# Kernel tuning notes

Measured on AMD Instinct MI355X. Metric: run time of the kernel, lower is better.

## Reference

```python
import jax, jax.numpy as jnp
import numpy as np

N = 100000
E = 3200000
NFEAT = 256
NHID = 256
NCLASS = 40


def _uniform(key, shape, stdv):
    return jax.random.uniform(key, shape, jnp.float32, -stdv, stdv)


def setup_inputs() -> dict:
    key = jax.random.key(0)
    ks = jax.random.split(key, 16)
    x = jax.random.normal(ks[0], (N, NFEAT), jnp.float32)
    edge_row = jax.random.randint(ks[1], (E,), 0, N, jnp.int32)
    edge_col = jax.random.randint(ks[2], (E,), 0, N, jnp.int32)
    edge_weight = jax.random.uniform(ks[3], (E,), jnp.float32)
    # MyLinear init: stdv = 1/sqrt(out_features)
    dims = [(NFEAT, NHID), (NHID, NHID), (NHID, NHID), (NHID, NCLASS)]
    params = {}
    for i, (fi, fo) in enumerate(dims):
        stdv = 1.0 / np.sqrt(fo)
        params[f"W{i+1}"] = _uniform(ks[4 + 2 * i], (fi, fo), stdv)
        params[f"b{i+1}"] = _uniform(ks[5 + 2 * i], (fo,), stdv)
    return dict(x=x, edge_row=edge_row, edge_col=edge_col, edge_weight=edge_weight, **params)


def _spmm(edge_row, edge_col, edge_weight, x):
    # out[i] = sum_{(i,j) in E} w_ij * x[j]
    msgs = edge_weight[:, None] * x[edge_col]  # [E, d]
    return jax.ops.segment_sum(msgs, edge_row, num_segments=N)


def reference(x, edge_row, edge_col, edge_weight, W1, b1, W2, b2, W3, b3, W4, b4):
    # layer 0 (ix % mlp_layers == 0 -> residual + spmm)
    h = x + _spmm(edge_row, edge_col, edge_weight, x)
    h = jax.nn.relu(h @ W1 + b1)
    # layer 1
    h = jax.nn.relu(h @ W2 + b2)
    # layer 2 (spmm + residual again)
    h = h + _spmm(edge_row, edge_col, edge_weight, h)
    h = jax.nn.relu(h @ W3 + b3)
    # layer 3 (final, no relu)
    h = h @ W4 + b4
    return jax.nn.log_softmax(h, axis=1)
```

## Files before the change

kernel.cpp:

```cpp
#include <hip/hip_runtime.h>
#include <hip/hip_bf16.h>
#include <cstdint>

#define N_NODES 100000
#define N_EDGES 3200000
#define NFEAT   256
#define NCLASS  40

#define BROWS_LOG 7
#define BROWS     128
#define NBUCK     782
#define CHUNK     8192
#define NBLK      391
#define GHN       (NBUCK * NBLK)

#define HP 264

typedef __bf16 bf16;
typedef __attribute__((ext_vector_type(8))) __bf16 bf16x8;
typedef __attribute__((ext_vector_type(4))) float f32x4;
typedef __attribute__((ext_vector_type(2))) float f32x2;

__device__ inline float b2f(unsigned short u) {
    union { unsigned int i; float f; } x; x.i = ((unsigned int)u) << 16; return x.f;
}
__device__ inline unsigned short f2b(float f) {
    union { float f; unsigned int i; } x; x.f = f;
    unsigned int i = x.i;
    return (unsigned short)((i + 0x7fffu + ((i >> 16) & 1u)) >> 16);
}
__device__ inline f32x2 unpack2(unsigned int d) {
    union { unsigned int i; float f; } lo, hi;
    lo.i = d << 16;
    hi.i = d & 0xFFFF0000u;
    return (f32x2){lo.f, hi.f};
}
__device__ inline unsigned int pack2(f32x2 a) {
    return ((unsigned int)f2b(a[0])) | (((unsigned int)f2b(a[1])) << 16);
}

__global__ void prep_w_kernel(const float* __restrict__ W1, const float* __restrict__ W2,
                              const float* __restrict__ W3, const float* __restrict__ W4,
                              unsigned short* __restrict__ WT1, unsigned short* __restrict__ WT2,
                              unsigned short* __restrict__ WT3, unsigned short* __restrict__ WT4) {
    int i = blockIdx.x * blockDim.x + threadIdx.x;
    if (i < 256 * 256) {
        int nIdx = i >> 8, k = i & 255;
        WT1[i] = f2b(W1[k * 256 + nIdx]);
        WT2[i] = f2b(W2[k * 256 + nIdx]);
        WT3[i] = f2b(W3[k * 256 + nIdx]);
    }
    if (i < 48 * 256) {
        int nIdx = i >> 8, k = i & 255;
        WT4[i] = (nIdx < NCLASS) ? f2b(W4[k * NCLASS + nIdx]) : (unsigned short)0;
    }
}

__global__ void cast_kernel(const float* __restrict__ X, unsigned short* __restrict__ Y, int n4) {
    int i = blockIdx.x * blockDim.x + threadIdx.x;
    if (i >= n4) return;
    float4 v = *(const float4*)(X + (size_t)i * 4);
    ushort4 o;
    o.x = f2b(v.x); o.y = f2b(v.y); o.z = f2b(v.z); o.w = f2b(v.w);
    *(ushort4*)(Y + (size_t)i * 4) = o;
}

__global__ __launch_bounds__(256) void p1a_kernel(const int* __restrict__ erow,
                                                  int* __restrict__ ghist) {
    __shared__ int h[NBUCK];
    for (int j = threadIdx.x; j < NBUCK; j += 256) h[j] = 0;
    __syncthreads();
    int base = blockIdx.x * CHUNK;
    for (int j = 0; j < CHUNK; j += 256) {
        int i = base + j + threadIdx.x;
        if (i < N_EDGES) atomicAdd(&h[erow[i] >> BROWS_LOG], 1);
    }
    __syncthreads();
    for (int j = threadIdx.x; j < NBUCK; j += 256)
        ghist[(size_t)j * NBLK + blockIdx.x] = h[j];
}

__global__ void scanB_blocks_kernel(int* __restrict__ g, int* __restrict__ bsums, int n) {
    __shared__ int s[1024];
    int i = blockIdx.x * 1024 + threadIdx.x;
    int v = (i < n) ? g[i] : 0;
    s[threadIdx.x] = v;
    __syncthreads();
    for (int off = 1; off < 1024; off <<= 1) {
        int t = (threadIdx.x >= off) ? s[threadIdx.x - off] : 0;
        __syncthreads();
        s[threadIdx.x] += t;
        __syncthreads();
    }
    if (i < n) g[i] = s[threadIdx.x] - v;
    if (threadIdx.x == 1023) bsums[blockIdx.x] = s[1023];
}

__global__ void scanB_sums_kernel(int* __restrict__ bsums, int nb) {
    __shared__ int s[512];
    int v = (threadIdx.x < nb) ? bsums[threadIdx.x] : 0;
    s[threadIdx.x] = v;
    __syncthreads();
    for (int off = 1; off < 512; off <<= 1) {
        int t = (threadIdx.x >= off) ? s[threadIdx.x - off] : 0;
        __syncthreads();
        s[threadIdx.x] += t;
        __syncthreads();
    }
    if (threadIdx.x < nb) bsums[threadIdx.x] = s[threadIdx.x] - v;
}

__global__ void scanB_add_kernel(int* __restrict__ g, const int* __restrict__ bsums, int n) {
    int i = blockIdx.x * blockDim.x + threadIdx.x;
    if (i < n) g[i] += bsums[i >> 10];
}

__global__ __launch_bounds__(256) void p1c_kernel(const int* __restrict__ erow,
                                                  const int* __restrict__ ecol,
                                                  const float* __restrict__ ew,
                                                  const int* __restrict__ ghist,
                                                  uint2* __restrict__ stage) {
    __shared__ int cur[NBUCK];
    for (int j = threadIdx.x; j < NBUCK; j += 256)
        cur[j] = ghist[(size_t)j * NBLK + blockIdx.x];
    __syncthreads();
    int base = blockIdx.x * CHUNK;
    for (int j = 0; j < CHUNK; j += 1024) {
        int r[4], c[4]; float w[4]; bool m[4];
#pragma unroll
        for (int q = 0; q < 4; q++) {
            int i = base + j + q * 256 + threadIdx.x;
            m[q] = (i < N_EDGES);
            if (m[q]) { r[q] = erow[i]; c[q] = ecol[i]; w[q] = ew[i]; }
        }
#pragma unroll
        for (int q = 0; q < 4; q++) {
            if (m[q]) {
                unsigned int qq = (unsigned int)(w[q] * 32768.f + 0.5f);
                if (qq > 32767u) qq = 32767u;
                int p = atomicAdd(&cur[r[q] >> BROWS_LOG], 1);
                stage[p] = make_uint2((unsigned int)r[q], (((unsigned int)c[q]) << 15) | qq);
            }
        }
    }
}

__global__ __launch_bounds__(256) void p2_kernel(const int* __restrict__ ghist,
                                                 const uint2* __restrict__ stage,
                                                 unsigned int* __restrict__ edges,
                                                 int* __restrict__ rowptr) {
    __shared__ int h[BROWS], sc[BROWS], lcur[BROWS];
    int b = blockIdx.x;
    int lo = ghist[(size_t)b * NBLK];
    int hi = (b + 1 < NBUCK) ? ghist[(size_t)(b + 1) * NBLK] : N_EDGES;
    if (threadIdx.x < BROWS) h[threadIdx.x] = 0;
    __syncthreads();
    for (int i = lo + threadIdx.x; i < hi; i += 256)
        atomicAdd(&h[stage[i].x & (BROWS - 1)], 1);
    __syncthreads();
    if (threadIdx.x < BROWS) sc[threadIdx.x] = h[threadIdx.x];
    __syncthreads();
    for (int off = 1; off < BROWS; off <<= 1) {
        int t = 0;
        if (threadIdx.x < BROWS && threadIdx.x >= off) t = sc[threadIdx.x - off];
        __syncthreads();
        if (threadIdx.x < BROWS) sc[threadIdx.x] += t;
        __syncthreads();
    }
    if (threadIdx.x < BROWS) {
        int ex = sc[threadIdx.x] - h[threadIdx.x];
        int row = b * BROWS + threadIdx.x;
        if (row <= N_NODES) rowptr[row] = lo + ex;
        lcur[threadIdx.x] = lo + ex;
    }
    __syncthreads();
    for (int i = lo + threadIdx.x; i < hi; i += 256) {
        uint2 sd = stage[i];
        int p = atomicAdd(&lcur[sd.x & (BROWS - 1)], 1);
        edges[p] = sd.y;
    }
}

__global__ void spmm_res_kernel(const unsigned short* __restrict__ X, unsigned short* __restrict__ Y,
                                const int* __restrict__ rowptr, const unsigned int* __restrict__ edges,
                                int n) {
    int gtid = blockIdx.x * blockDim.x + threadIdx.x;
    int row = gtid >> 6;
    int lane = gtid & 63;
    if (row >= n) return;
    const int half = lane >> 5;
    const int fb = (lane & 31) * 8;

    f32x2 acc[4];
    {
        uint4 xb = *(const uint4*)(X + (size_t)row * NFEAT + fb);
        if (half == 0) {
            acc[0] = unpack2(xb.x); acc[1] = unpack2(xb.y);
            acc[2] = unpack2(xb.z); acc[3] = unpack2(xb.w);
        } else {
            acc[0] = (f32x2){0.f, 0.f}; acc[1] = (f32x2){0.f, 0.f};
            acc[2] = (f32x2){0.f, 0.f}; acc[3] = (f32x2){0.f, 0.f};
        }
    }

    int s = rowptr[row], e = rowptr[row + 1];
    for (int k = s; k < e; k += 12) {
        int   c[6];
        f32x2 w2[6];
#pragma unroll
        for (int j = 0; j < 6; j++) {
            int kj = k + j * 2 + half;
            int kc = (kj < e) ? kj : (e - 1);
            unsigned int d = edges[kc];
            c[j] = (int)(d >> 15);
            float w = (kj < e) ? (float)(d & 32767u) * (1.f / 32768.f) : 0.f;
            w2[j] = (f32x2){w, w};
        }
        uint4 v[6];
#pragma unroll
        for (int j = 0; j < 6; j++) v[j] = *(const uint4*)(X + (size_t)c[j] * NFEAT + fb);
#pragma unroll
        for (int j = 0; j < 6; j++) {
            acc[0] += w2[j] * unpack2(v[j].x);
            acc[1] += w2[j] * unpack2(v[j].y);
            acc[2] += w2[j] * unpack2(v[j].z);
            acc[3] += w2[j] * unpack2(v[j].w);
        }
    }

#pragma unroll
    for (int i = 0; i < 4; i++) {
        acc[i][0] += __shfl_xor(acc[i][0], 32, 64);
        acc[i][1] += __shfl_xor(acc[i][1], 32, 64);
    }
    if (half == 0) {
        uint4 o;
        o.x = pack2(acc[0]); o.y = pack2(acc[1]);
        o.z = pack2(acc[2]); o.w = pack2(acc[3]);
        *(uint4*)(Y + (size_t)row * NFEAT + fb) = o;
    }
}

__global__ __launch_bounds__(256) void gemm12_kernel(
    const bf16* __restrict__ X,
    const bf16* __restrict__ WT1, const float* __restrict__ b1,
    const bf16* __restrict__ WT2, const float* __restrict__ b2,
    unsigned short* __restrict__ Y, int M) {
    __shared__ unsigned int sB[256 * 20];
    __shared__ unsigned short sH[64 * HP];
    const int tid = threadIdx.x;
    const int wave = tid >> 6;
    const int lane = tid & 63;
    const int m = lane & 15;
    const int quad = lane >> 4;
    const int lrow = wave * 16 + m;
    const int rowBase = blockIdx.x * 64;
    int arow = rowBase + lrow;
    if (arow >= M) arow = M - 1;

    f32x4 acc[16];
#pragma unroll
    for (int t = 0; t < 16; t++) acc[t] = (f32x4){0.f, 0.f, 0.f, 0.f};

    const bf16* xp = X + (size_t)arow * NFEAT + quad * 8;
#pragma unroll
    for (int k0 = 0; k0 < NFEAT; k0 += 32) {
#pragma unroll
        for (int f = tid; f < 1024; f += 256) {
            int n = f >> 2, j = f & 3;
            uint4 v = *(const uint4*)((const unsigned short*)WT1 + (size_t)n * NFEAT + k0 + j * 8);
            *(uint4*)&sB[n * 20 + j * 4] = v;
        }
        __syncthreads();
        bf16x8 a = *(const bf16x8*)(xp + k0);
#pragma unroll
        for (int t = 0; t < 16; t++) {
            bf16x8 b = *(const bf16x8*)&sB[(t * 16 + m) * 20 + quad * 4];
            acc[t] = __builtin_amdgcn_mfma_f32_16x16x32_bf16(b, a, acc[t], 0, 0, 0);
        }
        __syncthreads();
    }
#pragma unroll
    for (int t = 0; t < 16; t++) {
        const float* bp = b1 + t * 16 + quad * 4;
        f32x2 lo = (f32x2){fmaxf(acc[t][0] + bp[0], 0.f), fmaxf(acc[t][1] + bp[1], 0.f)};
        f32x2 hi = (f32x2){fmaxf(acc[t][2] + bp[2], 0.f), fmaxf(acc[t][3] + bp[3], 0.f)};
        *(uint2*)&sH[lrow * HP + t * 16 + quad * 4] = make_uint2(pack2(lo), pack2(hi));
        acc[t] = (f32x4){0.f, 0.f, 0.f, 0.f};
    }
    __syncthreads();

#pragma unroll
    for (int k0 = 0; k0 < NFEAT; k0 += 32) {
#pragma unroll
        for (int f = tid; f < 1024; f += 256) {
            int n = f >> 2, j = f & 3;
            uint4 v = *(const uint4*)((const unsigned short*)WT2 + (size_t)n * NFEAT + k0 + j * 8);
            *(uint4*)&sB[n * 20 + j * 4] = v;
        }
        __syncthreads();
        bf16x8 a = *(const bf16x8*)&sH[lrow * HP + k0 + quad * 8];
#pragma unroll
        for (int t = 0; t < 16; t++) {
            bf16x8 b = *(const bf16x8*)&sB[(t * 16 + m) * 20 + quad * 4];
            acc[t] = __builtin_amdgcn_mfma_f32_16x16x32_bf16(b, a, acc[t], 0, 0, 0);
        }
        __syncthreads();
    }
    const int row = rowBase + lrow;
    if (row < M) {
#pragma unroll
        for (int t = 0; t < 16; t++) {
            const float* bp = b2 + t * 16 + quad * 4;
            f32x2 lo = (f32x2){fmaxf(acc[t][0] + bp[0], 0.f), fmaxf(acc[t][1] + bp[1], 0.f)};
            f32x2 hi = (f32x2){fmaxf(acc[t][2] + bp[2], 0.f), fmaxf(acc[t][3] + bp[3], 0.f)};
            *(uint2*)(Y + (size_t)row * NFEAT + t * 16 + quad * 4) = make_uint2(pack2(lo), pack2(hi));
        }
    }
}

__global__ __launch_bounds__(256) void gemm34_ls_kernel(
    const bf16* __restrict__ X,
    const bf16* __restrict__ WT3, const float* __restrict__ b3,
    const bf16* __restrict__ WT4, const float* __restrict__ b4,
    float* __restrict__ out, int M) {
    __shared__ unsigned int sB[256 * 20];
    __shared__ unsigned short sH[64 * HP];
    const int tid = threadIdx.x;
    const int wave = tid >> 6;
    const int lane = tid & 63;
    const int m = lane & 15;
    const int quad = lane >> 4;
    const int lrow = wave * 16 + m;
    const int rowBase = blockIdx.x * 64;
    int arow = rowBase + lrow;
    if (arow >= M) arow = M - 1;

    f32x4 acc[16];
#pragma unroll
    for (int t = 0; t < 16; t++) acc[t] = (f32x4){0.f, 0.f, 0.f, 0.f};

    const bf16* xp = X + (size_t)arow * NFEAT + quad * 8;
#pragma unroll
    for (int k0 = 0; k0 < NFEAT; k0 += 32) {
#pragma unroll
        for (int f = tid; f < 1024; f += 256) {
            int n = f >> 2, j = f & 3;
            uint4 v = *(const uint4*)((const unsigned short*)WT3 + (size_t)n * NFEAT + k0 + j * 8);
            *(uint4*)&sB[n * 20 + j * 4] = v;
        }
        __syncthreads();
        bf16x8 a = *(const bf16x8*)(xp + k0);
#pragma unroll
        for (int t = 0; t < 16; t++) {
            bf16x8 b = *(const bf16x8*)&sB[(t * 16 + m) * 20 + quad * 4];
            acc[t] = __builtin_amdgcn_mfma_f32_16x16x32_bf16(b, a, acc[t], 0, 0, 0);
        }
        __syncthreads();
    }
#pragma unroll
    for (int t = 0; t < 16; t++) {
        const float* bp = b3 + t * 16 + quad * 4;
        f32x2 lo = (f32x2){fmaxf(acc[t][0] + bp[0], 0.f), fmaxf(acc[t][1] + bp[1], 0.f)};
        f32x2 hi = (f32x2){fmaxf(acc[t][2] + bp[2], 0.f), fmaxf(acc[t][3] + bp[3], 0.f)};
        *(uint2*)&sH[lrow * HP + t * 16 + quad * 4] = make_uint2(pack2(lo), pack2(hi));
    }
    __syncthreads();

    f32x4 a4[3];
#pragma unroll
    for (int t = 0; t < 3; t++) a4[t] = (f32x4){0.f, 0.f, 0.f, 0.f};
#pragma unroll
    for (int k0 = 0; k0 < NFEAT; k0 += 32) {
        if (tid < 192) {
            int n = tid >> 2, j = tid & 3;
            uint4 v = *(const uint4*)((const unsigned short*)WT4 + (size_t)n * NFEAT + k0 + j * 8);
            *(uint4*)&sB[n * 20 + j * 4] = v;
        }
        __syncthreads();
        bf16x8 a = *(const bf16x8*)&sH[lrow * HP + k0 + quad * 8];
#pragma unroll
        for (int t = 0; t < 3; t++) {
            bf16x8 b = *(const bf16x8*)&sB[(t * 16 + m) * 20 + quad * 4];
            a4[t] = __builtin_amdgcn_mfma_f32_16x16x32_bf16(b, a, a4[t], 0, 0, 0);
        }
        __syncthreads();
    }

    float v[3][4];
#pragma unroll
    for (int t = 0; t < 3; t++) {
        bool tv = (t < 2) || (quad < 2);
#pragma unroll
        for (int r = 0; r < 4; r++) {
            float bv = tv ? b4[t * 16 + quad * 4 + r] : 0.f;
            v[t][r] = tv ? (a4[t][r] + bv) : -1e30f;
        }
    }

    float mx = -1e30f;
#pragma unroll
    for (int t = 0; t < 3; t++)
#pragma unroll
        for (int r = 0; r < 4; r++) mx = fmaxf(mx, v[t][r]);
    mx = fmaxf(mx, __shfl_xor(mx, 16, 64));
    mx = fmaxf(mx, __shfl_xor(mx, 32, 64));

    float sm = 0.f;
#pragma unroll
    for (int t = 0; t < 3; t++) {
        bool tv = (t < 2) || (quad < 2);
        if (tv) {
#pragma unroll
            for (int r = 0; r < 4; r++) sm += __expf(v[t][r] - mx);
        }
    }
    sm += __shfl_xor(sm, 16, 64);
    sm += __shfl_xor(sm, 32, 64);
    float ls = __logf(sm);

    const int row = rowBase + lrow;
    if (row < M) {
#pragma unroll
        for (int t = 0; t < 3; t++) {
            if ((t < 2) || (quad < 2)) {
                f32x4 o = (f32x4){v[t][0] - mx - ls, v[t][1] - mx - ls,
                                  v[t][2] - mx - ls, v[t][3] - mx - ls};
                *(f32x4*)(out + (size_t)row * NCLASS + t * 16 + quad * 4) = o;
            }
        }
    }
}

extern "C" void kernel_launch(void* const* d_in, const int* in_sizes, int n_in,
                              void* d_out, int out_size, void* d_ws, size_t ws_size,
                              hipStream_t stream) {
    const float* x   = (const float*)d_in[0];
    const int* erow  = (const int*)d_in[1];
    const int* ecol  = (const int*)d_in[2];
    const float* ew  = (const float*)d_in[3];
    const float* W1  = (const float*)d_in[4];
    const float* W2  = (const float*)d_in[6];
    const float* W3  = (const float*)d_in[8];
    const float* W4  = (const float*)d_in[10];
    const float* b1  = (const float*)d_in[5];
    const float* b2  = (const float*)d_in[7];
    const float* b3  = (const float*)d_in[9];
    const float* b4  = (const float*)d_in[11];

    char* ws = (char*)d_ws;
    size_t off = 0;
    auto alloc = [&](size_t bytes) -> char* {
        char* p = ws + off;
        off = (off + bytes + 255) & ~(size_t)255;
        return p;
    };
    int* rowptr  = (int*)alloc((size_t)(N_NODES + 1) * 4);
    int* bsumsB  = (int*)alloc(512 * 4);
    unsigned int* edges = (unsigned int*)alloc((size_t)N_EDGES * 4);
    int* ghist   = (int*)alloc((size_t)GHN * 4);
    unsigned short* WT1 = (unsigned short*)alloc(256 * 256 * 2);
    unsigned short* WT2 = (unsigned short*)alloc(256 * 256 * 2);
    unsigned short* WT3 = (unsigned short*)alloc(256 * 256 * 2);
    unsigned short* WT4 = (unsigned short*)alloc(48 * 256 * 2);
    unsigned short* hA  = (unsigned short*)alloc((size_t)N_NODES * NFEAT * 2);
    uint2* stage        = (uint2*)hA;
    unsigned short* hB  = (unsigned short*)d_in[0];
    (void)ws_size; (void)n_in; (void)in_sizes; (void)out_size;

    prep_w_kernel<<<(256 * 256 + 255) / 256, 256, 0, stream>>>(
        W1, W2, W3, W4, WT1, WT2, WT3, WT4);
    p1a_kernel<<<NBLK, 256, 0, stream>>>(erow, ghist);
    int nsb = (GHN + 1023) / 1024;
    scanB_blocks_kernel<<<nsb, 1024, 0, stream>>>(ghist, bsumsB, GHN);
    scanB_sums_kernel<<<1, 512, 0, stream>>>(bsumsB, nsb);
    scanB_add_kernel<<<(GHN + 255) / 256, 256, 0, stream>>>(ghist, bsumsB, GHN);
    p1c_kernel<<<NBLK, 256, 0, stream>>>(erow, ecol, ew, ghist, stage);
    p2_kernel<<<NBUCK, 256, 0, stream>>>(ghist, stage, edges, rowptr);

    const int n4 = N_NODES * NFEAT / 4;
    const int spmm_grid = (N_NODES * 64 + 255) / 256;
    const int gemm_grid = (N_NODES + 63) / 64;

    cast_kernel<<<(n4 + 255) / 256, 256, 0, stream>>>(x, hA, n4);
    spmm_res_kernel<<<spmm_grid, 256, 0, stream>>>(hA, hB, rowptr, edges, N_NODES);
    gemm12_kernel<<<gemm_grid, 256, 0, stream>>>(
        (const bf16*)hB, (const bf16*)WT1, b1, (const bf16*)WT2, b2, hB, N_NODES);
    spmm_res_kernel<<<spmm_grid, 256, 0, stream>>>(hB, hA, rowptr, edges, N_NODES);
    gemm34_ls_kernel<<<gemm_grid, 256, 0, stream>>>(
        (const bf16*)hA, (const bf16*)WT3, b3, (const bf16*)WT4, b4, (float*)d_out, N_NODES);
}
```

Before: 917.2 us.

## Keep fused MLP intermediate in registers via permuted weight columns

The output columns of W1 and W3 (and their biases) are permuted at prep time so that each lane's MFMA accumulator layout already matches the A-operand fragment layout of the next GEMM. The intermediate hidden activations are then packed to bf16 in registers instead of being round-tripped through a padded shared-memory tile. This removes the sH buffer, one barrier and LDS traffic, and cuts shared memory per block. Launch bounds are raised to ask for 4 blocks per CU, which risks register spills given the 16 accumulators plus 8 held fragments.

```diff
diff --git a/kernel.cpp b/kernel.cpp
--- a/kernel.cpp
+++ b/kernel.cpp
@@ -14,8 +14,6 @@
 #define NBLK      391
 #define GHN       (NBUCK * NBLK)
 
-#define HP 264
-
 typedef __bf16 bf16;
 typedef __attribute__((ext_vector_type(8))) __bf16 bf16x8;
 typedef __attribute__((ext_vector_type(4))) float f32x4;
@@ -39,16 +37,24 @@
     return ((unsigned int)f2b(a[0])) | (((unsigned int)f2b(a[1])) << 16);
 }
 
+__host__ __device__ inline int permN(int s) {
+    return (((s >> 5) & 7) << 5) | (((s >> 2) & 3) << 3) | (((s >> 4) & 1) << 2) | (s & 3);
+}
+
 __global__ void prep_w_kernel(const float* __restrict__ W1, const float* __restrict__ W2,
                               const float* __restrict__ W3, const float* __restrict__ W4,
+                              const float* __restrict__ b1, const float* __restrict__ b3,
                               unsigned short* __restrict__ WT1, unsigned short* __restrict__ WT2,
-                              unsigned short* __restrict__ WT3, unsigned short* __restrict__ WT4) {
+                              unsigned short* __restrict__ WT3, unsigned short* __restrict__ WT4,
+                              float* __restrict__ b1p, float* __restrict__ b3p) {
     int i = blockIdx.x * blockDim.x + threadIdx.x;
     if (i < 256 * 256) {
-        int nIdx = i >> 8, k = i & 255;
-        WT1[i] = f2b(W1[k * 256 + nIdx]);
-        WT2[i] = f2b(W2[k * 256 + nIdx]);
-        WT3[i] = f2b(W3[k * 256 + nIdx]);
+        int s = i >> 8, k = i & 255;
+        int n = permN(s);
+        WT1[i] = f2b(W1[k * 256 + n]);
+        WT2[i] = f2b(W2[k * 256 + s]);
+        WT3[i] = f2b(W3[k * 256 + n]);
+        if (k == 0) { b1p[s] = b1[n]; b3p[s] = b3[n]; }
     }
     if (i < 48 * 256) {
         int nIdx = i >> 8, k = i & 255;
@@ -241,13 +247,12 @@
     }
 }
 
-__global__ __launch_bounds__(256) void gemm12_kernel(
+__global__ __launch_bounds__(256, 4) void gemm12_kernel(
     const bf16* __restrict__ X,
-    const bf16* __restrict__ WT1, const float* __restrict__ b1,
+    const bf16* __restrict__ WT1p, const float* __restrict__ b1p,
     const bf16* __restrict__ WT2, const float* __restrict__ b2,
     unsigned short* __restrict__ Y, int M) {
     __shared__ unsigned int sB[256 * 20];
-    __shared__ unsigned short sH[64 * HP];
     const int tid = threadIdx.x;
     const int wave = tid >> 6;
     const int lane = tid & 63;
@@ -268,7 +273,7 @@
 #pragma unroll
         for (int f = tid; f < 1024; f += 256) {
             int n = f >> 2, j = f & 3;
-            uint4 v = *(const uint4*)((const unsigned short*)WT1 + (size_t)n * NFEAT + k0 + j * 8);
+            uint4 v = *(const uint4*)((const unsigned short*)WT1p + (size_t)n * NFEAT + k0 + j * 8);
             *(uint4*)&sB[n * 20 + j * 4] = v;
         }
         __syncthreads();
@@ -280,15 +285,25 @@
         }
         __syncthreads();
     }
-#pragma unroll
-    for (int t = 0; t < 16; t++) {
-        const float* bp = b1 + t * 16 + quad * 4;
-        f32x2 lo = (f32x2){fmaxf(acc[t][0] + bp[0], 0.f), fmaxf(acc[t][1] + bp[1], 0.f)};
-        f32x2 hi = (f32x2){fmaxf(acc[t][2] + bp[2], 0.f), fmaxf(acc[t][3] + bp[3], 0.f)};
-        *(uint2*)&sH[lrow * HP + t * 16 + quad * 4] = make_uint2(pack2(lo), pack2(hi));
-        acc[t] = (f32x4){0.f, 0.f, 0.f, 0.f};
-    }
-    __syncthreads();
+
+    bf16x8 af[8];
+#pragma unroll
+    for (int kc = 0; kc < 8; kc++) {
+        const float* p0 = b1p + (2 * kc) * 16 + quad * 4;
+        const float* p1 = b1p + (2 * kc + 1) * 16 + quad * 4;
+        union { unsigned int u[4]; bf16x8 h; } cv;
+        cv.u[0] = pack2((f32x2){fmaxf(acc[2 * kc][0] + p0[0], 0.f),
+                                fmaxf(acc[2 * kc][1] + p0[1], 0.f)});
+        cv.u[1] = pack2((f32x2){fmaxf(acc[2 * kc][2] + p0[2], 0.f),
+                                fmaxf(acc[2 * kc][3] + p0[3], 0.f)});
+        cv.u[2] = pack2((f32x2){fmaxf(acc[2 * kc + 1][0] + p1[0], 0.f),
+                                fmaxf(acc[2 * kc + 1][1] + p1[1], 0.f)});
+        cv.u[3] = pack2((f32x2){fmaxf(acc[2 * kc + 1][2] + p1[2], 0.f),
+                                fmaxf(acc[2 * kc + 1][3] + p1[3], 0.f)});
+        af[kc] = cv.h;
+        acc[2 * kc] = (f32x4){0.f, 0.f, 0.f, 0.f};
+        acc[2 * kc + 1] = (f32x4){0.f, 0.f, 0.f, 0.f};
+    }
 
 #pragma unroll
     for (int k0 = 0; k0 < NFEAT; k0 += 32) {
@@ -299,7 +314,7 @@
             *(uint4*)&sB[n * 20 + j * 4] = v;
         }
         __syncthreads();
-        bf16x8 a = *(const bf16x8*)&sH[lrow * HP + k0 + quad * 8];
+        bf16x8 a = af[k0 >> 5];
 #pragma unroll
         for (int t = 0; t < 16; t++) {
             bf16x8 b = *(const bf16x8*)&sB[(t * 16 + m) * 20 + quad * 4];
@@ -319,13 +334,12 @@
     }
 }
 
-__global__ __launch_bounds__(256) void gemm34_ls_kernel(
+__global__ __launch_bounds__(256, 4) void gemm34_ls_kernel(
     const bf16* __restrict__ X,
-    const bf16* __restrict__ WT3, const float* __restrict__ b3,
+    const bf16* __restrict__ WT3p, const float* __restrict__ b3p,
     const bf16* __restrict__ WT4, const float* __restrict__ b4,
     float* __restrict__ out, int M) {
     __shared__ unsigned int sB[256 * 20];
-    __shared__ unsigned short sH[64 * HP];
     const int tid = threadIdx.x;
     const int wave = tid >> 6;
     const int lane = tid & 63;
@@ -346,7 +360,7 @@
 #pragma unroll
         for (int f = tid; f < 1024; f += 256) {
             int n = f >> 2, j = f & 3;
-            uint4 v = *(const uint4*)((const unsigned short*)WT3 + (size_t)n * NFEAT + k0 + j * 8);
+            uint4 v = *(const uint4*)((const unsigned short*)WT3p + (size_t)n * NFEAT + k0 + j * 8);
             *(uint4*)&sB[n * 20 + j * 4] = v;
         }
         __syncthreads();
@@ -358,14 +372,23 @@
         }
         __syncthreads();
     }
-#pragma unroll
-    for (int t = 0; t < 16; t++) {
-        const float* bp = b3 + t * 16 + quad * 4;
-        f32x2 lo = (f32x2){fmaxf(acc[t][0] + bp[0], 0.f), fmaxf(acc[t][1] + bp[1], 0.f)};
-        f32x2 hi = (f32x2){fmaxf(acc[t][2] + bp[2], 0.f), fmaxf(acc[t][3] + bp[3], 0.f)};
-        *(uint2*)&sH[lrow * HP + t * 16 + quad * 4] = make_uint2(pack2(lo), pack2(hi));
-    }
-    __syncthreads();
+
+    bf16x8 af[8];
+#pragma unroll
+    for (int kc = 0; kc < 8; kc++) {
+        const float* p0 = b3p + (2 * kc) * 16 + quad * 4;
+        const float* p1 = b3p + (2 * kc + 1) * 16 + quad * 4;
+        union { unsigned int u[4]; bf16x8 h; } cv;
+        cv.u[0] = pack2((f32x2){fmaxf(acc[2 * kc][0] + p0[0], 0.f),
+                                fmaxf(acc[2 * kc][1] + p0[1], 0.f)});
+        cv.u[1] = pack2((f32x2){fmaxf(acc[2 * kc][2] + p0[2], 0.f),
+                                fmaxf(acc[2 * kc][3] + p0[3], 0.f)});
+        cv.u[2] = pack2((f32x2){fmaxf(acc[2 * kc + 1][0] + p1[0], 0.f),
+                                fmaxf(acc[2 * kc + 1][1] + p1[1], 0.f)});
+        cv.u[3] = pack2((f32x2){fmaxf(acc[2 * kc + 1][2] + p1[2], 0.f),
+                                fmaxf(acc[2 * kc + 1][3] + p1[3], 0.f)});
+        af[kc] = cv.h;
+    }
 
     f32x4 a4[3];
 #pragma unroll
@@ -378,7 +401,7 @@
             *(uint4*)&sB[n * 20 + j * 4] = v;
         }
         __syncthreads();
-        bf16x8 a = *(const bf16x8*)&sH[lrow * HP + k0 + quad * 8];
+        bf16x8 a = af[k0 >> 5];
 #pragma unroll
         for (int t = 0; t < 3; t++) {
             bf16x8 b = *(const bf16x8*)&sB[(t * 16 + m) * 20 + quad * 4];
@@ -463,13 +486,15 @@
     unsigned short* WT2 = (unsigned short*)alloc(256 * 256 * 2);
     unsigned short* WT3 = (unsigned short*)alloc(256 * 256 * 2);
     unsigned short* WT4 = (unsigned short*)alloc(48 * 256 * 2);
+    float* b1p          = (float*)alloc(256 * 4);
+    float* b3p          = (float*)alloc(256 * 4);
     unsigned short* hA  = (unsigned short*)alloc((size_t)N_NODES * NFEAT * 2);
     uint2* stage        = (uint2*)hA;
     unsigned short* hB  = (unsigned short*)d_in[0];
     (void)ws_size; (void)n_in; (void)in_sizes; (void)out_size;
 
     prep_w_kernel<<<(256 * 256 + 255) / 256, 256, 0, stream>>>(
-        W1, W2, W3, W4, WT1, WT2, WT3, WT4);
+        W1, W2, W3, W4, b1, b3, WT1, WT2, WT3, WT4, b1p, b3p);
     p1a_kernel<<<NBLK, 256, 0, stream>>>(erow, ghist);
     int nsb = (GHN + 1023) / 1024;
     scanB_blocks_kernel<<<nsb, 1024, 0, stream>>>(ghist, bsumsB, GHN);
@@ -485,8 +510,8 @@
     cast_kernel<<<(n4 + 255) / 256, 256, 0, stream>>>(x, hA, n4);
     spmm_res_kernel<<<spmm_grid, 256, 0, stream>>>(hA, hB, rowptr, edges, N_NODES);
     gemm12_kernel<<<gemm_grid, 256, 0, stream>>>(
-        (const bf16*)hB, (const bf16*)WT1, b1, (const bf16*)WT2, b2, hB, N_NODES);
+        (const bf16*)hB, (const bf16*)WT1, b1p, (const bf16*)WT2, b2, hB, N_NODES);
     spmm_res_kernel<<<spmm_grid, 256, 0, stream>>>(hB, hA, rowptr, edges, N_NODES);
     gemm34_ls_kernel<<<gemm_grid, 256, 0, stream>>>(
-        (const bf16*)hA, (const bf16*)WT3, b3, (const bf16*)WT4, b4, (float*)d_out, N_NODES);
-}
+        (const bf16*)hA, (const bf16*)WT3, b3p, (const bf16*)WT4, b4, (float*)d_out, N_NODES);
+}
```

After: 928.6 us. About the same (+1.3%).
